# Performance work log

Measured on AMD Instinct MI355X. Metric: run time of the kernel, lower is better.

Reference implementation:

```python
import jax, jax.numpy as jnp
import numpy as np

N = 1048576        # number of time samples (rays)
V = 32             # num_videos
D = 32             # embedding_dim
F = 6              # num_frequencies
K = 2 * F + 1      # basis size: [1, sin(2^j*pi*t), cos(2^j*pi*t)]


def setup_inputs() -> dict:
    key = jax.random.key(0)
    k1, k2, k3 = jax.random.split(key, 3)
    times = jax.random.uniform(k1, (N, 1), dtype=jnp.float32)
    video_ids = jax.random.randint(k2, (N, 1), 0, V, dtype=jnp.int32)
    weights = jax.random.normal(k3, (V, D, K), dtype=jnp.float32)
    return {"times": times, "video_ids": video_ids, "weights": weights}


def _fourier_basis(t):
    # t: [N] -> [N, K] with basis [1, sin(2^j pi t), cos(2^j pi t)] j=0..F-1
    freqs = (2.0 ** jnp.arange(F, dtype=t.dtype)) * jnp.pi  # [F]
    ang = t[:, None] * freqs                                # [N, F]
    return jnp.concatenate(
        [jnp.ones_like(t)[:, None], jnp.sin(ang), jnp.cos(ang)], axis=-1
    )


def reference(times, video_ids, weights):
    shp = times.shape
    t = times.reshape(-1)                       # [N]
    vid = video_ids.reshape(-1).astype(jnp.int32)  # [N]
    basis = _fourier_basis(t)                   # [N, K]
    w = weights[vid]                            # gather: [N, D, K]
    emb = jnp.einsum('ndk,nk->nd', w, basis)    # [N, D]
    return emb.reshape((*shp[:-1], -1))
```

## Files before the change

### kernel.cpp

```cpp
#include <hip/hip_runtime.h>
#include <hip/hip_fp16.h>

#define NRAYS 1048576
#define NV 32
#define ND 32
#define NF 6
#define NK 13

typedef _Float16 h2 __attribute__((ext_vector_type(2)));
typedef float f4 __attribute__((ext_vector_type(4)));

__device__ __forceinline__ float fdot2acc(h2 a, h2 b, float c) {
#if __has_builtin(__builtin_amdgcn_fdot2)
    return __builtin_amdgcn_fdot2(a, b, c, false);
#else
    return c + (float)a.x * (float)b.x + (float)a.y * (float)b.y;
#endif
}

__device__ __forceinline__ h2 pack2(float a, float b) {
#if __has_builtin(__builtin_amdgcn_cvt_pkrtz)
    return __builtin_bit_cast(h2, __builtin_amdgcn_cvt_pkrtz(a, b));
#else
    h2 r; r.x = (_Float16)a; r.y = (_Float16)b; return r;
#endif
}

__device__ __forceinline__ float hwsin(float rev) {
#if __has_builtin(__builtin_amdgcn_sinf)
    return __builtin_amdgcn_sinf(rev);
#else
    return __sinf(6.28318530717958647692f * rev);
#endif
}
__device__ __forceinline__ float hwcos(float rev) {
#if __has_builtin(__builtin_amdgcn_cosf)
    return __builtin_amdgcn_cosf(rev);
#else
    return __cosf(6.28318530717958647692f * rev);
#endif
}

__device__ __forceinline__ void make_basis(float t, h2 bp[7]) {
    float sv[NF], cv[NF];
    sv[0] = hwsin(0.5f * t);
    cv[0] = hwcos(0.5f * t);
#pragma unroll
    for (int j = 1; j < NF; ++j) {
        float sj = sv[j - 1], cj = cv[j - 1];
        sv[j] = 2.f * sj * cj;
        cv[j] = fmaf(-2.f * sj, sj, 1.f);
    }
    bp[0] = pack2(1.0f, sv[0]);
    bp[1] = pack2(sv[1], sv[2]);
    bp[2] = pack2(sv[3], sv[4]);
    bp[3] = pack2(sv[5], cv[0]);
    bp[4] = pack2(cv[1], cv[2]);
    bp[5] = pack2(cv[3], cv[4]);
    bp[6] = pack2(cv[5], 0.0f);
}

__global__ void pack_weights_kernel(const float* __restrict__ weights,
                                    unsigned* __restrict__ wpack)
{
    int j = blockIdx.x * 256 + threadIdx.x;
    if (j >= NV * 7 * 32) return;
    int v = j / 224;
    int r = j - v * 224;
    int i = r >> 5;
    int c = r & 31;
    int pos = c >> 2;
    int e = c & 3;
    int q = pos ^ (v & 7);
    int d = 4 * q + e;
    float w0 = weights[v * (ND * NK) + d * NK + 2 * i];
    float w1 = (2 * i + 1 < NK) ? weights[v * (ND * NK) + d * NK + 2 * i + 1] : 0.f;
    wpack[j] = __builtin_bit_cast(unsigned, pack2(w0, w1));
}

__global__ __launch_bounds__(256, 5) void VideoEmbedding_kernel(
    const float* __restrict__ times,
    const int* __restrict__ vids,
    const unsigned* __restrict__ wpack,
    float* __restrict__ out)
{
    __shared__ _Float16 wl[NV * 7 * ND * 2];
    __shared__ float s_t[512];
    __shared__ unsigned char s_v[512];

    const int tid = threadIdx.x;
    const int rbase = blockIdx.x * 512;

    uint4 wst[7];
    {
        const uint4* src = reinterpret_cast<const uint4*>(wpack);
#pragma unroll
        for (int j = 0; j < 7; ++j)
            wst[j] = src[tid + j * 256];
    }
    const float t0 = times[rbase + tid];
    const float t1 = times[rbase + 256 + tid];
    const int v0i = vids[rbase + tid];
    const int v1i = vids[rbase + 256 + tid];

    {
        uint4* dst = reinterpret_cast<uint4*>(wl);
#pragma unroll
        for (int j = 0; j < 7; ++j)
            dst[tid + j * 256] = wst[j];
    }
    s_t[tid] = t0;
    s_t[tid + 256] = t1;
    s_v[tid] = (unsigned char)v0i;
    s_v[tid + 256] = (unsigned char)v1i;
    __syncthreads();

    const int q = tid & 7;
    const int g = tid >> 3;

    uint4 wA[7], wB[7];
    {
        const int v = s_v[g];
        const unsigned b = (unsigned)v * 448u + (unsigned)(q ^ (v & 7)) * 8u;
#pragma unroll
        for (int i = 0; i < 7; ++i)
            wA[i] = *reinterpret_cast<const uint4*>(&wl[b + i * 64]);
    }

#define ITER(P, WCUR, WNEXT)                                                  \
    {                                                                         \
        if ((P) < 15) {                    \
            const int nv = s_v[((P) + 1) * 32 + g];                           \
            const unsigned nb =                                               \
                (unsigned)nv * 448u + (unsigned)(q ^ (nv & 7)) * 8u;          \
            _Pragma("unroll")                                                 \
            for (int i = 0; i < 7; ++i)                                       \
                WNEXT[i] = *reinterpret_cast<const uint4*>(&wl[nb + i * 64]); \
        }                                                                     \
        const float t = s_t[(P) * 32 + g];                                    \
        h2 bp[7];                                                             \
        make_basis(t, bp);                                                    \
        float a0 = 0.f, a1 = 0.f, a2 = 0.f, a3 = 0.f;                         \
        _Pragma("unroll")                                                     \
        for (int i = 0; i < 7; ++i) {                                         \
            a0 = fdot2acc(__builtin_bit_cast(h2, WCUR[i].x), bp[i], a0);      \
            a1 = fdot2acc(__builtin_bit_cast(h2, WCUR[i].y), bp[i], a1);      \
            a2 = fdot2acc(__builtin_bit_cast(h2, WCUR[i].z), bp[i], a2);      \
            a3 = fdot2acc(__builtin_bit_cast(h2, WCUR[i].w), bp[i], a3);      \
        }                                                                     \
        f4 res;                                                               \
        res.x = a0; res.y = a1; res.z = a2; res.w = a3;                       \
        reinterpret_cast<f4*>(out)[(size_t)(rbase + (P) * 32 + g) * 8 + q] =  \
            res;                                                              \
    }

    for (int p = 0; p < 16; p += 2) {
        ITER(p, wA, wB)
        ITER(p + 1, wB, wA)
    }
#undef ITER
}

extern "C" void kernel_launch(void* const* d_in, const int* in_sizes, int n_in,
                              void* d_out, int out_size, void* d_ws, size_t ws_size,
                              hipStream_t stream) {
    const float* times = (const float*)d_in[0];
    const int* vids = (const int*)d_in[1];
    const float* weights = (const float*)d_in[2];
    float* out = (float*)d_out;
    unsigned* wpack = (unsigned*)d_ws;

    hipLaunchKernelGGL(pack_weights_kernel, dim3(28), dim3(256), 0, stream,
                       weights, wpack);
    hipLaunchKernelGGL(VideoEmbedding_kernel, dim3(2048), dim3(256), 0, stream,
                       times, vids, wpack, out);
}
```

Measured before the change: 33.77 us.

## Compute Fourier basis once per ray into LDS instead of per lane

Each ray's Fourier basis was previously recomputed by all 8 lanes that share that ray. Now each thread computes the basis for one ray, packs it as fp16 pairs and stores it in shared memory, and the main loop reads it back. The block size in rays is halved to 256, so there are 4096 blocks, and the occupancy hint drops from 5 to 4. The cost is that every block reloads the full 28 KB weight table into LDS, which now happens twice as often, plus the extra LDS traffic for the basis.

Result: no change. 34.34 us (+1.7%).

```diff
diff --git a/kernel.cpp b/kernel.cpp
--- a/kernel.cpp
+++ b/kernel.cpp
@@ -41,25 +41,6 @@
 #endif
 }
 
-__device__ __forceinline__ void make_basis(float t, h2 bp[7]) {
-    float sv[NF], cv[NF];
-    sv[0] = hwsin(0.5f * t);
-    cv[0] = hwcos(0.5f * t);
-#pragma unroll
-    for (int j = 1; j < NF; ++j) {
-        float sj = sv[j - 1], cj = cv[j - 1];
-        sv[j] = 2.f * sj * cj;
-        cv[j] = fmaf(-2.f * sj, sj, 1.f);
-    }
-    bp[0] = pack2(1.0f, sv[0]);
-    bp[1] = pack2(sv[1], sv[2]);
-    bp[2] = pack2(sv[3], sv[4]);
-    bp[3] = pack2(sv[5], cv[0]);
-    bp[4] = pack2(cv[1], cv[2]);
-    bp[5] = pack2(cv[3], cv[4]);
-    bp[6] = pack2(cv[5], 0.0f);
-}
-
 __global__ void pack_weights_kernel(const float* __restrict__ weights,
                                     unsigned* __restrict__ wpack)
 {
@@ -78,18 +59,18 @@
     wpack[j] = __builtin_bit_cast(unsigned, pack2(w0, w1));
 }
 
-__global__ __launch_bounds__(256, 5) void VideoEmbedding_kernel(
+__global__ __launch_bounds__(256, 4) void VideoEmbedding_kernel(
     const float* __restrict__ times,
     const int* __restrict__ vids,
     const unsigned* __restrict__ wpack,
     float* __restrict__ out)
 {
     __shared__ _Float16 wl[NV * 7 * ND * 2];
-    __shared__ float s_t[512];
-    __shared__ unsigned char s_v[512];
+    __shared__ unsigned s_bp[256 * 8];
+    __shared__ unsigned char s_v[256];
 
     const int tid = threadIdx.x;
-    const int rbase = blockIdx.x * 512;
+    const int rbase = blockIdx.x * 256;
 
     uint4 wst[7];
     {
@@ -98,10 +79,8 @@
         for (int j = 0; j < 7; ++j)
             wst[j] = src[tid + j * 256];
     }
-    const float t0 = times[rbase + tid];
-    const float t1 = times[rbase + 256 + tid];
-    const int v0i = vids[rbase + tid];
-    const int v1i = vids[rbase + 256 + tid];
+    const float t = times[rbase + tid];
+    const int vid = vids[rbase + tid];
 
     {
         uint4* dst = reinterpret_cast<uint4*>(wl);
@@ -109,10 +88,30 @@
         for (int j = 0; j < 7; ++j)
             dst[tid + j * 256] = wst[j];
     }
-    s_t[tid] = t0;
-    s_t[tid + 256] = t1;
-    s_v[tid] = (unsigned char)v0i;
-    s_v[tid + 256] = (unsigned char)v1i;
+    s_v[tid] = (unsigned char)vid;
+
+    {
+        float sv[NF], cv[NF];
+        sv[0] = hwsin(0.5f * t);
+        cv[0] = hwcos(0.5f * t);
+#pragma unroll
+        for (int j = 1; j < NF; ++j) {
+            float sj = sv[j - 1], cj = cv[j - 1];
+            sv[j] = 2.f * sj * cj;
+            cv[j] = fmaf(-2.f * sj, sj, 1.f);
+        }
+        uint4 lo, hi;
+        lo.x = __builtin_bit_cast(unsigned, pack2(1.0f, sv[0]));
+        lo.y = __builtin_bit_cast(unsigned, pack2(sv[1], sv[2]));
+        lo.z = __builtin_bit_cast(unsigned, pack2(sv[3], sv[4]));
+        lo.w = __builtin_bit_cast(unsigned, pack2(sv[5], cv[0]));
+        hi.x = __builtin_bit_cast(unsigned, pack2(cv[1], cv[2]));
+        hi.y = __builtin_bit_cast(unsigned, pack2(cv[3], cv[4]));
+        hi.z = __builtin_bit_cast(unsigned, pack2(cv[5], 0.0f));
+        hi.w = 0u;
+        reinterpret_cast<uint4*>(s_bp)[tid * 2] = lo;
+        reinterpret_cast<uint4*>(s_bp)[tid * 2 + 1] = hi;
+    }
     __syncthreads();
 
     const int q = tid & 7;
@@ -129,7 +128,7 @@
 
 #define ITER(P, WCUR, WNEXT)                                                  \
     {                                                                         \
-        if ((P) < 15) {                    \
+        if ((P) < 7) {                     \
             const int nv = s_v[((P) + 1) * 32 + g];                           \
             const unsigned nb =                                               \
                 (unsigned)nv * 448u + (unsigned)(q ^ (nv & 7)) * 8u;          \
@@ -137,9 +136,17 @@
             for (int i = 0; i < 7; ++i)                                       \
                 WNEXT[i] = *reinterpret_cast<const uint4*>(&wl[nb + i * 64]); \
         }                                                                     \
-        const float t = s_t[(P) * 32 + g];                                    \
+        const int slot = (P) * 32 + g;                                        \
+        const uint4 bpa = reinterpret_cast<const uint4*>(s_bp)[slot * 2];     \
+        const uint4 bpb = reinterpret_cast<const uint4*>(s_bp)[slot * 2 + 1]; \
         h2 bp[7];                                                             \
-        make_basis(t, bp);                                                    \
+        bp[0] = __builtin_bit_cast(h2, bpa.x);                                \
+        bp[1] = __builtin_bit_cast(h2, bpa.y);                                \
+        bp[2] = __builtin_bit_cast(h2, bpa.z);                                \
+        bp[3] = __builtin_bit_cast(h2, bpa.w);                                \
+        bp[4] = __builtin_bit_cast(h2, bpb.x);                                \
+        bp[5] = __builtin_bit_cast(h2, bpb.y);                                \
+        bp[6] = __builtin_bit_cast(h2, bpb.z);                                \
         float a0 = 0.f, a1 = 0.f, a2 = 0.f, a3 = 0.f;                         \
         _Pragma("unroll")                                                     \
         for (int i = 0; i < 7; ++i) {                                         \
@@ -150,11 +157,10 @@
         }                                                                     \
         f4 res;                                                               \
         res.x = a0; res.y = a1; res.z = a2; res.w = a3;                       \
-        reinterpret_cast<f4*>(out)[(size_t)(rbase + (P) * 32 + g) * 8 + q] =  \
-            res;                                                              \
+        reinterpret_cast<f4*>(out)[(size_t)(rbase + slot) * 8 + q] = res;     \
     }
 
-    for (int p = 0; p < 16; p += 2) {
+    for (int p = 0; p < 8; p += 2) {
         ITER(p, wA, wB)
         ITER(p + 1, wB, wA)
     }
@@ -172,6 +178,6 @@
 
     hipLaunchKernelGGL(pack_weights_kernel, dim3(28), dim3(256), 0, stream,
                        weights, wpack);
-    hipLaunchKernelGGL(VideoEmbedding_kernel, dim3(2048), dim3(256), 0, stream,
+    hipLaunchKernelGGL(VideoEmbedding_kernel, dim3(4096), dim3(256), 0, stream,
                        times, vids, wpack, out);
 }
```
